# Optimization experiments

Measured on AMD Instinct MI355X. Metric: run time of the kernel, lower is better.

The kernel has to match this reference:

```python
import jax, jax.numpy as jnp
import numpy as np

VOCAB = 1_000_000
B, F, E = 16384, 39, 16
LAYERS = [200, 200, 200]


def setup_inputs() -> dict:
    key = jax.random.key(0)
    ks = jax.random.split(key, 12)
    feat_ids = jax.random.randint(ks[0], (B, F), 0, VOCAB)
    feat_vals = jnp.ones((B, F), dtype=jnp.float32)
    # xavier-ish init for tables and MLP weights
    w = jax.random.normal(ks[1], (VOCAB, 1), dtype=jnp.float32) * 0.01
    v = jax.random.normal(ks[2], (VOCAB, E), dtype=jnp.float32) * 0.01
    b = jnp.zeros((1,), dtype=jnp.float32)
    params = {}
    node_in = E
    for i, h in enumerate(LAYERS):
        scale = (2.0 / (node_in + h)) ** 0.5
        params[f'w{i}'] = jax.random.normal(ks[3 + i], (node_in, h), dtype=jnp.float32) * scale
        params[f'b{i}'] = jnp.zeros((h,), dtype=jnp.float32)
        node_in = h
    return dict(feat_ids=feat_ids, feat_vals=feat_vals, w=w, v=v, b=b,
                w0=params['w0'], b0=params['b0'],
                w1=params['w1'], b1=params['b1'],
                w2=params['w2'], b2=params['b2'])


def reference(feat_ids, feat_vals, w, v, b, w0, b0, w1, b1, w2, b2):
    # X @ v  (sparse one-hot matmul == embedding gather + weighted sum over fields)
    ve = v[feat_ids]                                   # [B, F, E]
    xv = jnp.einsum('bf,bfe->be', feat_vals, ve)       # [B, E]
    # X^2 @ v^2
    x2v2 = jnp.einsum('bf,bfe->be', feat_vals * feat_vals, ve * ve)  # [B, E]
    fm = 0.5 * (xv * xv - x2v2)                        # [B, E]
    # MLP (dropout in test mode: keep_prob = 1 -> identity)
    h = jax.nn.relu(fm @ w0 + b0)
    h = jax.nn.relu(h @ w1 + b1)
    h = jax.nn.relu(h @ w2 + b2)
    bilinear = jnp.sum(h, axis=1, keepdims=True)       # [B, 1]
    # LR part: X @ w
    lr = jnp.einsum('bf,bfo->bo', feat_vals, w[feat_ids])  # [B, 1]
    logits = jnp.reshape(lr + b + bilinear, (-1,))     # [B]
    return jax.nn.sigmoid(logits)
```

## Files before the change

kernel.cpp:

```cpp
#include <hip/hip_runtime.h>
#include <math.h>

#define NFM_B 16384
#define NFM_F 39
#define NFM_E 16
#define NFM_H 200
#define TR    8
#define KPAD  232
#define NT    13
#define VOCAB 1000000

typedef short short8   __attribute__((ext_vector_type(8)));
typedef short short4_t __attribute__((ext_vector_type(4)));
typedef float floatx4  __attribute__((ext_vector_type(4)));

__device__ __forceinline__ short f2bf(float x) {
    union { float f; unsigned u; } a; a.f = x;
    unsigned r = a.u + 0x7FFF + ((a.u >> 16) & 1);
    return (short)(r >> 16);
}
__device__ __forceinline__ float bf2f(short s) {
    union { unsigned u; float f; } a;
    a.u = ((unsigned)(unsigned short)s) << 16;
    return a.f;
}

#define WBF_SZ   VOCAB
#define FRAG_OFF WBF_SZ
#define W0F_OFF  0
#define W0F_SZ   (NT * 1 * 64 * 8)
#define W1F_OFF  (W0F_OFF + W0F_SZ)
#define W1F_SZ   (NT * 7 * 64 * 8)
#define W2F_OFF  (W1F_OFF + W1F_SZ)
#define W2F_SZ   (NT * 7 * 64 * 8)
#define WS_FRAGS (W2F_OFF + W2F_SZ)
#define FRAG_BLOCKS  ((WS_FRAGS + 255) / 256)
#define WCONV_THREADS (VOCAB / 8)
#define WCONV_BLOCKS ((WCONV_THREADS + 255) / 256)

__global__ __launch_bounds__(256)
void nfm_prep_kernel(const float* __restrict__ w,
                     const float* __restrict__ w0,
                     const float* __restrict__ w1,
                     const float* __restrict__ w2,
                     short* __restrict__ ws)
{
    if (blockIdx.x < FRAG_BLOCKS) {
        const int idx = blockIdx.x * 256 + threadIdx.x;
        if (idx >= WS_FRAGS) return;
        float val;
        if (idx < W1F_OFF) {
            const int rem = idx;
            const int j = rem & 7, lane = (rem >> 3) & 63, tile = rem >> 9;
            const int k = (lane >> 4) * 8 + j;
            const int n = tile * 16 + (lane & 15);
            val = (k < NFM_E && n < NFM_H) ? w0[k * NFM_H + n] : 0.f;
        } else if (idx < W2F_OFF) {
            const int rem = idx - W1F_OFF;
            const int j = rem & 7, lane = (rem >> 3) & 63;
            const int kt = rem >> 9;
            const int ks = kt % 7, tile = kt / 7;
            const int k = ks * 32 + (lane >> 4) * 8 + j;
            const int n = tile * 16 + (lane & 15);
            val = (k < NFM_H && n < NFM_H) ? w1[k * NFM_H + n] : 0.f;
        } else {
            const int rem = idx - W2F_OFF;
            const int j = rem & 7, lane = (rem >> 3) & 63;
            const int kt = rem >> 9;
            const int ks = kt % 7, tile = kt / 7;
            const int k = ks * 32 + (lane >> 4) * 8 + j;
            const int n = tile * 16 + (lane & 15);
            val = (k < NFM_H && n < NFM_H) ? w2[k * NFM_H + n] : 0.f;
        }
        ws[FRAG_OFF + idx] = f2bf(val);
    } else {
        const int t = (blockIdx.x - FRAG_BLOCKS) * 256 + threadIdx.x;
        if (t >= WCONV_THREADS) return;
        const int base = t * 8;
        const float4 a = *(const float4*)&w[base];
        const float4 b = *(const float4*)&w[base + 4];
        short8 o;
        o[0] = f2bf(a.x); o[1] = f2bf(a.y); o[2] = f2bf(a.z); o[3] = f2bf(a.w);
        o[4] = f2bf(b.x); o[5] = f2bf(b.y); o[6] = f2bf(b.z); o[7] = f2bf(b.w);
        *(short8*)&ws[base] = o;
    }
}

__global__ __launch_bounds__(256, 8)
void nfm_main_kernel(
    const int*   __restrict__ feat_ids,
    const float* __restrict__ feat_vals,
    const float* __restrict__ v,
    const float* __restrict__ bglob,
    const float* __restrict__ b0,
    const float* __restrict__ b1,
    const float* __restrict__ b2,
    const short* __restrict__ ws,
    float* __restrict__ out)
{
    __shared__ __attribute__((aligned(16))) short hbfA[16 * KPAD];
    __shared__ __attribute__((aligned(16))) short hbfB[16 * KPAD];
    __shared__ float rowsumW[4][16];
    __shared__ float lrS[TR];

    const int tid  = threadIdx.x;
    const int row0 = blockIdx.x * TR;
    const int lane = tid & 63;
    const int wv   = tid >> 6;
    const int lq   = lane >> 4;
    const int ln   = lane & 15;

    const short* wbf = ws;
    const short* Wfb = ws + FRAG_OFF;

    const int r8  = tid >> 5;
    const int l32 = tid & 31;
    const int fs  = l32 >> 2, eg = l32 & 3;
    const long rbase = (long)(row0 + r8) * NFM_F;

    int   idv[5]; float vlv[5];
#pragma unroll
    for (int it = 0; it < 5; ++it) {
        const int f = fs + it * 8;
        const bool ok = f < NFM_F;
        idv[it] = ok ? feat_ids [rbase + f] : 0;
        vlv[it] = ok ? feat_vals[rbase + f] : 0.f;
    }
    float4 ve[5];
#pragma unroll
    for (int it = 0; it < 5; ++it)
        ve[it] = *(const float4*)&v[(long)idv[it] * NFM_E + eg * 4];

    const int   idw1 = feat_ids [rbase + l32];
    const float vw1  = feat_vals[rbase + l32];
    const int   idw2 = (l32 < 7) ? feat_ids [rbase + 32 + l32] : 0;
    const float vw2  = (l32 < 7) ? feat_vals[rbase + 32 + l32] : 0.f;
    const float wv1  = bf2f(wbf[idw1]);
    const float wv2  = bf2f(wbf[idw2]);

    {
        short8 z8 = {0, 0, 0, 0, 0, 0, 0, 0};
        short8* pA = (short8*)hbfA;
        short8* pB = (short8*)hbfB;
        for (int i = tid; i < 464; i += 256) { pA[i] = z8; pB[i] = z8; }
    }
    __syncthreads();

    {
        floatx4 xv = {0.f, 0.f, 0.f, 0.f}, x2 = {0.f, 0.f, 0.f, 0.f};
#pragma unroll
        for (int it = 0; it < 5; ++it) {
            const float val = vlv[it];
            const float t0 = val * ve[it].x, t1 = val * ve[it].y;
            const float t2 = val * ve[it].z, t3 = val * ve[it].w;
            xv[0] += t0; xv[1] += t1; xv[2] += t2; xv[3] += t3;
            x2[0] = fmaf(t0, t0, x2[0]); x2[1] = fmaf(t1, t1, x2[1]);
            x2[2] = fmaf(t2, t2, x2[2]); x2[3] = fmaf(t3, t3, x2[3]);
        }
#pragma unroll
        for (int off = 4; off <= 16; off <<= 1) {
#pragma unroll
            for (int c = 0; c < 4; ++c) {
                xv[c] += __shfl_xor(xv[c], off, 32);
                x2[c] += __shfl_xor(x2[c], off, 32);
            }
        }
        if (fs == 0) {
            short4_t fm4;
#pragma unroll
            for (int c = 0; c < 4; ++c)
                fm4[c] = f2bf(0.5f * (xv[c] * xv[c] - x2[c]));
            *(short4_t*)&hbfB[r8 * KPAD + eg * 4] = fm4;
        }
        float lr = vw1 * wv1 + vw2 * wv2;
#pragma unroll
        for (int off = 16; off >= 1; off >>= 1)
            lr += __shfl_xor(lr, off, 32);
        if (l32 == 0) lrS[r8] = lr;
    }
    __syncthreads();

    {
        const short8 af = *(const short8*)&hbfB[ln * KPAD + lq * 8];
        const short* Wf = Wfb + W0F_OFF;
        for (int t = wv; t < NT; t += 4) {
            const int n = t * 16 + ln;
            const float bj = (n < NFM_H) ? b0[n] : 0.f;
            floatx4 acc = {bj, bj, bj, bj};
            const short8 bf = *(const short8*)&Wf[(t * 64 + lane) * 8];
            acc = __builtin_amdgcn_mfma_f32_16x16x32_bf16(af, bf, acc, 0, 0, 0);
#pragma unroll
            for (int rg = 0; rg < 4; ++rg)
                hbfA[(lq * 4 + rg) * KPAD + n] = f2bf(fmaxf(acc[rg], 0.f));
        }
    }
    __syncthreads();

    {
        short8 af[7];
#pragma unroll
        for (int ks = 0; ks < 7; ++ks)
            af[ks] = *(const short8*)&hbfA[ln * KPAD + ks * 32 + lq * 8];
        const short* Wf = Wfb + W1F_OFF;
        for (int t = wv; t < NT; t += 4) {
            const int n = t * 16 + ln;
            const float bj = (n < NFM_H) ? b1[n] : 0.f;
            floatx4 acc = {bj, bj, bj, bj};
#pragma unroll
            for (int ks = 0; ks < 7; ++ks) {
                const short8 bf = *(const short8*)&Wf[((t * 7 + ks) * 64 + lane) * 8];
                acc = __builtin_amdgcn_mfma_f32_16x16x32_bf16(af[ks], bf, acc, 0, 0, 0);
            }
#pragma unroll
            for (int rg = 0; rg < 4; ++rg)
                hbfB[(lq * 4 + rg) * KPAD + n] = f2bf(fmaxf(acc[rg], 0.f));
        }
    }
    __syncthreads();

    {
        short8 af[7];
#pragma unroll
        for (int ks = 0; ks < 7; ++ks)
            af[ks] = *(const short8*)&hbfB[ln * KPAD + ks * 32 + lq * 8];
        const short* Wf = Wfb + W2F_OFF;
        float rs[4] = {0.f, 0.f, 0.f, 0.f};
        for (int t = wv; t < NT; t += 4) {
            const int n = t * 16 + ln;
            const float bj = (n < NFM_H) ? b2[n] : 0.f;
            floatx4 acc = {bj, bj, bj, bj};
#pragma unroll
            for (int ks = 0; ks < 7; ++ks) {
                const short8 bf = *(const short8*)&Wf[((t * 7 + ks) * 64 + lane) * 8];
                acc = __builtin_amdgcn_mfma_f32_16x16x32_bf16(af[ks], bf, acc, 0, 0, 0);
            }
#pragma unroll
            for (int rg = 0; rg < 4; ++rg)
                rs[rg] += fmaxf(acc[rg], 0.f);
        }
#pragma unroll
        for (int off = 8; off >= 1; off >>= 1)
#pragma unroll
            for (int rg = 0; rg < 4; ++rg)
                rs[rg] += __shfl_xor(rs[rg], off, 16);
        if (ln == 0)
#pragma unroll
            for (int rg = 0; rg < 4; ++rg)
                rowsumW[wv][lq * 4 + rg] = rs[rg];
    }
    __syncthreads();

    if (tid < TR) {
        const float s = rowsumW[0][tid] + rowsumW[1][tid]
                      + rowsumW[2][tid] + rowsumW[3][tid];
        const float logit = lrS[tid] + bglob[0] + s;
        out[row0 + tid] = 1.f / (1.f + expf(-logit));
    }
}

extern "C" void kernel_launch(void* const* d_in, const int* in_sizes, int n_in,
                              void* d_out, int out_size, void* d_ws, size_t ws_size,
                              hipStream_t stream) {
    const int*   feat_ids  = (const int*)  d_in[0];
    const float* feat_vals = (const float*)d_in[1];
    const float* w   = (const float*)d_in[2];
    const float* v   = (const float*)d_in[3];
    const float* b   = (const float*)d_in[4];
    const float* w0  = (const float*)d_in[5];
    const float* b0  = (const float*)d_in[6];
    const float* w1  = (const float*)d_in[7];
    const float* b1  = (const float*)d_in[8];
    const float* w2  = (const float*)d_in[9];
    const float* b2  = (const float*)d_in[10];
    float* out = (float*)d_out;
    short* ws  = (short*)d_ws;

    hipLaunchKernelGGL(nfm_prep_kernel, dim3(FRAG_BLOCKS + WCONV_BLOCKS), dim3(256),
                       0, stream, w, w0, w1, w2, ws);
    hipLaunchKernelGGL(nfm_main_kernel, dim3(NFM_B / TR), dim3(256), 0, stream,
                       feat_ids, feat_vals, v, b, b0, b1, b2, ws, out);
}
```

Before: 139.8 us.

## Drop bf16 LR table conversion and gather fp32 w directly in main kernel

```diff
diff --git a/kernel.cpp b/kernel.cpp
--- a/kernel.cpp
+++ b/kernel.cpp
@@ -5,7 +5,7 @@
 #define NFM_F 39
 #define NFM_E 16
 #define NFM_H 200
-#define TR    8
+#define TR    16
 #define KPAD  232
 #define NT    13
 #define VOCAB 1000000
@@ -19,14 +19,7 @@
     unsigned r = a.u + 0x7FFF + ((a.u >> 16) & 1);
     return (short)(r >> 16);
 }
-__device__ __forceinline__ float bf2f(short s) {
-    union { unsigned u; float f; } a;
-    a.u = ((unsigned)(unsigned short)s) << 16;
-    return a.f;
-}
-
-#define WBF_SZ   VOCAB
-#define FRAG_OFF WBF_SZ
+
 #define W0F_OFF  0
 #define W0F_SZ   (NT * 1 * 64 * 8)
 #define W1F_OFF  (W0F_OFF + W0F_SZ)
@@ -35,62 +28,48 @@
 #define W2F_SZ   (NT * 7 * 64 * 8)
 #define WS_FRAGS (W2F_OFF + W2F_SZ)
 #define FRAG_BLOCKS  ((WS_FRAGS + 255) / 256)
-#define WCONV_THREADS (VOCAB / 8)
-#define WCONV_BLOCKS ((WCONV_THREADS + 255) / 256)
 
 __global__ __launch_bounds__(256)
-void nfm_prep_kernel(const float* __restrict__ w,
-                     const float* __restrict__ w0,
+void nfm_prep_kernel(const float* __restrict__ w0,
                      const float* __restrict__ w1,
                      const float* __restrict__ w2,
                      short* __restrict__ ws)
 {
-    if (blockIdx.x < FRAG_BLOCKS) {
-        const int idx = blockIdx.x * 256 + threadIdx.x;
-        if (idx >= WS_FRAGS) return;
-        float val;
-        if (idx < W1F_OFF) {
-            const int rem = idx;
-            const int j = rem & 7, lane = (rem >> 3) & 63, tile = rem >> 9;
-            const int k = (lane >> 4) * 8 + j;
-            const int n = tile * 16 + (lane & 15);
-            val = (k < NFM_E && n < NFM_H) ? w0[k * NFM_H + n] : 0.f;
-        } else if (idx < W2F_OFF) {
-            const int rem = idx - W1F_OFF;
-            const int j = rem & 7, lane = (rem >> 3) & 63;
-            const int kt = rem >> 9;
-            const int ks = kt % 7, tile = kt / 7;
-            const int k = ks * 32 + (lane >> 4) * 8 + j;
-            const int n = tile * 16 + (lane & 15);
-            val = (k < NFM_H && n < NFM_H) ? w1[k * NFM_H + n] : 0.f;
-        } else {
-            const int rem = idx - W2F_OFF;
-            const int j = rem & 7, lane = (rem >> 3) & 63;
-            const int kt = rem >> 9;
-            const int ks = kt % 7, tile = kt / 7;
-            const int k = ks * 32 + (lane >> 4) * 8 + j;
-            const int n = tile * 16 + (lane & 15);
-            val = (k < NFM_H && n < NFM_H) ? w2[k * NFM_H + n] : 0.f;
-        }
-        ws[FRAG_OFF + idx] = f2bf(val);
+    const int idx = blockIdx.x * 256 + threadIdx.x;
+    if (idx >= WS_FRAGS) return;
+    float val;
+    if (idx < W1F_OFF) {
+        const int rem = idx;
+        const int j = rem & 7, lane = (rem >> 3) & 63, tile = rem >> 9;
+        const int k = (lane >> 4) * 8 + j;
+        const int n = tile * 16 + (lane & 15);
+        val = (k < NFM_E && n < NFM_H) ? w0[k * NFM_H + n] : 0.f;
+    } else if (idx < W2F_OFF) {
+        const int rem = idx - W1F_OFF;
+        const int j = rem & 7, lane = (rem >> 3) & 63;
+        const int kt = rem >> 9;
+        const int ks = kt % 7, tile = kt / 7;
+        const int k = ks * 32 + (lane >> 4) * 8 + j;
+        const int n = tile * 16 + (lane & 15);
+        val = (k < NFM_H && n < NFM_H) ? w1[k * NFM_H + n] : 0.f;
     } else {
-        const int t = (blockIdx.x - FRAG_BLOCKS) * 256 + threadIdx.x;
-        if (t >= WCONV_THREADS) return;
-        const int base = t * 8;
-        const float4 a = *(const float4*)&w[base];
-        const float4 b = *(const float4*)&w[base + 4];
-        short8 o;
-        o[0] = f2bf(a.x); o[1] = f2bf(a.y); o[2] = f2bf(a.z); o[3] = f2bf(a.w);
-        o[4] = f2bf(b.x); o[5] = f2bf(b.y); o[6] = f2bf(b.z); o[7] = f2bf(b.w);
-        *(short8*)&ws[base] = o;
-    }
-}
-
-__global__ __launch_bounds__(256, 8)
+        const int rem = idx - W2F_OFF;
+        const int j = rem & 7, lane = (rem >> 3) & 63;
+        const int kt = rem >> 9;
+        const int ks = kt % 7, tile = kt / 7;
+        const int k = ks * 32 + (lane >> 4) * 8 + j;
+        const int n = tile * 16 + (lane & 15);
+        val = (k < NFM_H && n < NFM_H) ? w2[k * NFM_H + n] : 0.f;
+    }
+    ws[idx] = f2bf(val);
+}
+
+__global__ __launch_bounds__(256, 4)
 void nfm_main_kernel(
     const int*   __restrict__ feat_ids,
     const float* __restrict__ feat_vals,
     const float* __restrict__ v,
+    const float* __restrict__ w,
     const float* __restrict__ bglob,
     const float* __restrict__ b0,
     const float* __restrict__ b1,
@@ -110,33 +89,28 @@
     const int lq   = lane >> 4;
     const int ln   = lane & 15;
 
-    const short* wbf = ws;
-    const short* Wfb = ws + FRAG_OFF;
-
-    const int r8  = tid >> 5;
-    const int l32 = tid & 31;
-    const int fs  = l32 >> 2, eg = l32 & 3;
-    const long rbase = (long)(row0 + r8) * NFM_F;
-
-    int   idv[5]; float vlv[5];
-#pragma unroll
-    for (int it = 0; it < 5; ++it) {
-        const int f = fs + it * 8;
+    const short* Wfb = ws;
+
+    const int rr  = tid >> 4;
+    const int l16 = tid & 15;
+    const int eg  = l16 & 3;
+    const int fs  = l16 >> 2;
+    const long rbase = (long)(row0 + rr) * NFM_F;
+
+    int   idv[10]; float vlv[10];
+#pragma unroll
+    for (int it = 0; it < 10; ++it) {
+        const int f = fs + it * 4;
         const bool ok = f < NFM_F;
         idv[it] = ok ? feat_ids [rbase + f] : 0;
         vlv[it] = ok ? feat_vals[rbase + f] : 0.f;
     }
-    float4 ve[5];
-#pragma unroll
-    for (int it = 0; it < 5; ++it)
+    float4 ve[10]; float wg[10];
+#pragma unroll
+    for (int it = 0; it < 10; ++it) {
         ve[it] = *(const float4*)&v[(long)idv[it] * NFM_E + eg * 4];
-
-    const int   idw1 = feat_ids [rbase + l32];
-    const float vw1  = feat_vals[rbase + l32];
-    const int   idw2 = (l32 < 7) ? feat_ids [rbase + 32 + l32] : 0;
-    const float vw2  = (l32 < 7) ? feat_vals[rbase + 32 + l32] : 0.f;
-    const float wv1  = bf2f(wbf[idw1]);
-    const float wv2  = bf2f(wbf[idw2]);
+        wg[it] = w[idv[it]];
+    }
 
     {
         short8 z8 = {0, 0, 0, 0, 0, 0, 0, 0};
@@ -149,7 +123,7 @@
     {
         floatx4 xv = {0.f, 0.f, 0.f, 0.f}, x2 = {0.f, 0.f, 0.f, 0.f};
 #pragma unroll
-        for (int it = 0; it < 5; ++it) {
+        for (int it = 0; it < 10; ++it) {
             const float val = vlv[it];
             const float t0 = val * ve[it].x, t1 = val * ve[it].y;
             const float t2 = val * ve[it].z, t3 = val * ve[it].w;
@@ -158,11 +132,11 @@
             x2[2] = fmaf(t2, t2, x2[2]); x2[3] = fmaf(t3, t3, x2[3]);
         }
 #pragma unroll
-        for (int off = 4; off <= 16; off <<= 1) {
+        for (int off = 4; off <= 8; off <<= 1) {
 #pragma unroll
             for (int c = 0; c < 4; ++c) {
-                xv[c] += __shfl_xor(xv[c], off, 32);
-                x2[c] += __shfl_xor(x2[c], off, 32);
+                xv[c] += __shfl_xor(xv[c], off, 16);
+                x2[c] += __shfl_xor(x2[c], off, 16);
             }
         }
         if (fs == 0) {
@@ -170,13 +144,16 @@
 #pragma unroll
             for (int c = 0; c < 4; ++c)
                 fm4[c] = f2bf(0.5f * (xv[c] * xv[c] - x2[c]));
-            *(short4_t*)&hbfB[r8 * KPAD + eg * 4] = fm4;
-        }
-        float lr = vw1 * wv1 + vw2 * wv2;
-#pragma unroll
-        for (int off = 16; off >= 1; off >>= 1)
-            lr += __shfl_xor(lr, off, 32);
-        if (l32 == 0) lrS[r8] = lr;
+            *(short4_t*)&hbfB[rr * KPAD + eg * 4] = fm4;
+        }
+        float lr = 0.f;
+#pragma unroll
+        for (int it = 0; it < 10; ++it)
+            lr = fmaf(vlv[it], wg[it], lr);
+        lr = (eg == 0) ? lr : 0.f;
+        lr += __shfl_xor(lr, 4, 16);
+        lr += __shfl_xor(lr, 8, 16);
+        if (l16 == 0) lrS[rr] = lr;
     }
     __syncthreads();
 
@@ -275,8 +252,8 @@
     float* out = (float*)d_out;
     short* ws  = (short*)d_ws;
 
-    hipLaunchKernelGGL(nfm_prep_kernel, dim3(FRAG_BLOCKS + WCONV_BLOCKS), dim3(256),
-                       0, stream, w, w0, w1, w2, ws);
+    hipLaunchKernelGGL(nfm_prep_kernel, dim3(FRAG_BLOCKS), dim3(256),
+                       0, stream, w0, w1, w2, ws);
     hipLaunchKernelGGL(nfm_main_kernel, dim3(NFM_B / TR), dim3(256), 0, stream,
-                       feat_ids, feat_vals, v, b, b0, b1, b2, ws, out);
-}
+                       feat_ids, feat_vals, v, w, b, b0, b1, b2, ws, out);
+}
```

Result: faster. 133.3 us (-4.7%).
